# Optimization experiments

Measured on AMD Instinct MI355X. Metric: run time of the kernel, lower is better.

## Reference

```python
import jax, jax.numpy as jnp
import numpy as np

NUM_NODES = 200000
NUM_EDGES = 640000
RANK = 16
EMBED_DIM = 128


def setup_inputs() -> dict:
    key = jax.random.key(0)
    k1, k2, k3 = jax.random.split(key, 3)
    U = jax.random.normal(k1, (NUM_NODES, RANK), dtype=jnp.float32)
    V = jax.random.normal(k2, (RANK, EMBED_DIM), dtype=jnp.float32)
    edge_index = jax.random.randint(k3, (2, NUM_EDGES), 0, NUM_NODES, dtype=jnp.int64)
    return {"U": U, "V": V, "edge_index": edge_index}


def reference(U, V, edge_index):
    # Low-rank projection: [N, r] @ [r, d] -> [N, d]
    embeddings = jnp.matmul(U, V)
    src, dst = edge_index[0], edge_index[1]
    # Mean aggregation (PyG MessagePassing aggr='mean', source_to_target):
    # gather messages from source nodes, segment-mean into destination nodes.
    msgs = embeddings[src]  # [E, d]
    summed = jax.ops.segment_sum(msgs, dst, num_segments=NUM_NODES)  # [N, d]
    counts = jax.ops.segment_sum(jnp.ones((edge_index.shape[1],), dtype=embeddings.dtype),
                                 dst, num_segments=NUM_NODES)  # [N]
    denom = jnp.maximum(counts, 1.0)  # isolated nodes -> 0 output (scatter-mean semantics)
    return summed / denom[:, None]
```

## Files before the change

### kernel.cpp

```cpp
#include <hip/hip_runtime.h>

#define RANK 16
#define EMBED_DIM 128
#define CAP 16

typedef float floatx4 __attribute__((ext_vector_type(4)));

__global__ __launch_bounds__(256) void fill_slots(
        const int* __restrict__ eiw,
        int* __restrict__ cnt,
        int* __restrict__ ovfcnt,
        int* __restrict__ slots,
        int* __restrict__ ovf,
        int E, int nwords) {
    __shared__ int iflag;
    if (threadIdx.x == 0) iflag = 0;
    __syncthreads();
    {
        int w = 2 * threadIdx.x + 1;
        unsigned int v = (w < nwords) ? ((const unsigned int*)eiw)[w] : 0u;
        if (v) atomicOr(&iflag, 1);
    }
    __syncthreads();
    const bool is32 = (iflag != 0);

    const int base = (blockIdx.x * 256 + threadIdx.x) * 2;
    if (base >= E) return;

    int srcs[2], dsts[2];
    int ne;
    if ((E & 1) == 0 && base + 1 < E) {
        ne = 2;
        if (is32) {
            int2 s = *(const int2*)(eiw + base);
            int2 d = *(const int2*)(eiw + E + base);
            srcs[0] = s.x; srcs[1] = s.y;
            dsts[0] = d.x; dsts[1] = d.y;
        } else {
            int4 sv = *(const int4*)(eiw + 2 * base);
            int4 dv = *(const int4*)(eiw + 2 * (E + base));
            srcs[0] = sv.x; srcs[1] = sv.z;
            dsts[0] = dv.x; dsts[1] = dv.z;
        }
    } else {
        ne = 0;
        for (int e = base; e < E && e < base + 2; ++e, ++ne) {
            srcs[ne] = is32 ? eiw[e] : eiw[2 * e];
            dsts[ne] = is32 ? eiw[E + e] : eiw[2 * (E + e)];
        }
    }

#pragma unroll
    for (int j = 0; j < 2; ++j) {
        if (j >= ne) break;
        int dst = dsts[j];
        int pos = atomicAdd(&cnt[dst], 1);
        if (pos < CAP) {
            slots[(size_t)dst * CAP + pos] = srcs[j];
        } else {
            int o = atomicAdd(ovfcnt, 1);
            ovf[2 * o]     = srcs[j];
            ovf[2 * o + 1] = dst;
        }
    }
}

__global__ __launch_bounds__(256) void gather_project(
        const float* __restrict__ U,
        const float* __restrict__ V,
        const int* __restrict__ cnt,
        const int* __restrict__ slots,
        const int* __restrict__ ovfcnt,
        const int* __restrict__ ovf,
        float* __restrict__ out, int N, int ntiles) {
    __shared__ float4 Vs4[RANK * EMBED_DIM / 4];
    __shared__ float accs[32][RANK];
    __shared__ float sinv[32];
    __shared__ int   scnt[32];
    __shared__ int4  sslot4[32 * CAP / 4];

    const int t = threadIdx.x;
    const float4* V4 = (const float4*)V;
    Vs4[t]       = V4[t];
    Vs4[t + 256] = V4[t + 256];

    const int g = t >> 4;
    const int j = t & 15;
    const int q = t & 31;
    const int w = t >> 5;
    const int* sslot = (const int*)sslot4;

    for (int tile = blockIdx.x; tile < ntiles; tile += gridDim.x) {
        const int n0 = tile * 32;
        __syncthreads();

        if (t < 32) {
            int n = n0 + t;
            int c = (n < N) ? cnt[n] : 0;
            scnt[t] = c;
            sinv[t] = 1.0f / fmaxf((float)c, 1.0f);
        }
        if (t < 128) {
            const int4* g4 = (const int4*)(slots + (size_t)n0 * CAP);
            if (n0 + (t >> 2) < N) sslot4[t] = g4[t];
        }
        __syncthreads();

#pragma unroll
        for (int half = 0; half < 2; ++half) {
            int nd = half * 16 + g;
            int n = n0 + nd;
            float acc = 0.f;
            if (n < N) {
                int deg = scnt[nd];
                int k = deg < CAP ? deg : CAP;
                const int* sl = sslot + nd * CAP;
                for (int e = 0; e < k; e += 4) {
                    int s0 = sl[e];
                    int s1 = (e + 1 < k) ? sl[e + 1] : s0;
                    int s2 = (e + 2 < k) ? sl[e + 2] : s0;
                    int s3 = (e + 3 < k) ? sl[e + 3] : s0;
                    float u0 = U[(size_t)s0 * RANK + j];
                    float u1 = U[(size_t)s1 * RANK + j];
                    float u2 = U[(size_t)s2 * RANK + j];
                    float u3 = U[(size_t)s3 * RANK + j];
                    acc += u0;
                    acc += (e + 1 < k) ? u1 : 0.f;
                    acc += (e + 2 < k) ? u2 : 0.f;
                    acc += (e + 3 < k) ? u3 : 0.f;
                }
                if (deg > CAP) {
                    int m = *ovfcnt;
                    for (int i = 0; i < m; ++i)
                        if (ovf[2 * i + 1] == n)
                            acc += U[(size_t)ovf[2 * i] * RANK + j];
                }
            }
            accs[nd][j] = acc;
        }
        __syncthreads();

#pragma unroll
        for (int r = 0; r < 4; ++r) {
            int nd = 4 * w + r;
            float4 a4 = make_float4(0.f, 0.f, 0.f, 0.f);
#pragma unroll
            for (int k = 0; k < RANK; ++k) {
                float a = accs[nd][k];
                float4 v = Vs4[k * 32 + q];
                a4.x = fmaf(a, v.x, a4.x);
                a4.y = fmaf(a, v.y, a4.y);
                a4.z = fmaf(a, v.z, a4.z);
                a4.w = fmaf(a, v.w, a4.w);
            }
            float s = sinv[nd];
            int n = n0 + nd;
            if (n < N) {
                floatx4 o;
                o.x = a4.x * s; o.y = a4.y * s; o.z = a4.z * s; o.w = a4.w * s;
                __builtin_nontemporal_store(
                    o, (floatx4*)out + (size_t)n * (EMBED_DIM / 4) + q);
            }
        }
    }
}

extern "C" void kernel_launch(void* const* d_in, const int* in_sizes, int n_in,
                              void* d_out, int out_size, void* d_ws, size_t ws_size,
                              hipStream_t stream) {
    const float* U = (const float*)d_in[0];
    const float* V = (const float*)d_in[1];
    const int* EI = (const int*)d_in[2];
    float* out = (float*)d_out;

    const int N = in_sizes[0] / RANK;
    const int E = in_sizes[2] / 2;
    const int nwords = in_sizes[2];

    int* wsI = (int*)d_ws;
    int* cnt = wsI;
    int* ovfcnt = wsI + N;
    const int slots_off = (N + 1 + 15) & ~15;
    int* slots = wsI + slots_off;
    int* ovf = slots + (size_t)N * CAP;

    (void)hipMemsetAsync(d_ws, 0, (size_t)(N + 1) * sizeof(int), stream);

    fill_slots<<<(E / 2 + 255) / 256, 256, 0, stream>>>(
        EI, cnt, ovfcnt, slots, ovf, E, nwords);

    const int ntiles = (N + 31) / 32;
    const int nblk = ntiles < 2560 ? ntiles : 2560;
    gather_project<<<nblk, 256, 0, stream>>>(
        U, V, cnt, slots, ovfcnt, ovf, out, N, ntiles);
}
```

Before: 180.4 us.

## Vectorize U-row gathers with float4 loads and shuffle-reduce, 64 nodes per block

The gather phase now has each thread load a float4 quarter of a U row. Four edges per node are processed in parallel by 16 lanes, and the partial sums are combined with xor shuffles. This replaces the old scalar per-lane loads and aims to cut load instruction count and raise memory-level parallelism. The persistent grid-stride loop is replaced by one 64-node tile per block, with a larger grid. This drops loop overhead and syncthreads per tile, but it reloads V into shared memory in every block.

Result: faster. 173.2 us, median of 2 (-4.0%).

```diff
diff --git a/kernel.cpp b/kernel.cpp
--- a/kernel.cpp
+++ b/kernel.cpp
@@ -5,6 +5,15 @@
 #define CAP 16
 
 typedef float floatx4 __attribute__((ext_vector_type(4)));
+
+__device__ inline floatx4 shflx4(floatx4 v, int mask) {
+    floatx4 r;
+    r.x = __shfl_xor(v.x, mask);
+    r.y = __shfl_xor(v.y, mask);
+    r.z = __shfl_xor(v.z, mask);
+    r.w = __shfl_xor(v.w, mask);
+    return r;
+}
 
 __global__ __launch_bounds__(256) void fill_slots(
         const int* __restrict__ eiw,
@@ -72,95 +81,93 @@
         const int* __restrict__ slots,
         const int* __restrict__ ovfcnt,
         const int* __restrict__ ovf,
-        float* __restrict__ out, int N, int ntiles) {
-    __shared__ float4 Vs4[RANK * EMBED_DIM / 4];
-    __shared__ float accs[32][RANK];
-    __shared__ float sinv[32];
-    __shared__ int   scnt[32];
-    __shared__ int4  sslot4[32 * CAP / 4];
+        float* __restrict__ out, int N) {
+    __shared__ float4  Vs4[RANK * EMBED_DIM / 4];
+    __shared__ floatx4 accs4[64][4];
+    __shared__ float   sinv[64];
+    __shared__ int     scnt[64];
+    __shared__ int4    sslot4[64 * CAP / 4];
 
     const int t = threadIdx.x;
     const float4* V4 = (const float4*)V;
     Vs4[t]       = V4[t];
     Vs4[t + 256] = V4[t + 256];
 
-    const int g = t >> 4;
-    const int j = t & 15;
+    const int n0 = blockIdx.x * 64;
+
+    if (t < 64) {
+        int n = n0 + t;
+        int c = (n < N) ? cnt[n] : 0;
+        scnt[t] = c;
+        sinv[t] = 1.0f / fmaxf((float)c, 1.0f);
+    }
+    {
+        const int4* g4 = (const int4*)(slots + (size_t)n0 * CAP);
+        if (n0 + (t >> 2) < N) sslot4[t] = g4[t];
+    }
+    __syncthreads();
+
+    const int* sslot = (const int*)sslot4;
+    const int g    = t >> 4;
+    const int l    = t & 15;
+    const int es   = l >> 2;
+    const int quad = l & 3;
+
+#pragma unroll
+    for (int half = 0; half < 4; ++half) {
+        int nd = half * 16 + g;
+        int n = n0 + nd;
+        int deg = scnt[nd];
+        int k = deg < CAP ? deg : CAP;
+        const int* sl = sslot + nd * CAP;
+        floatx4 a = (floatx4)0.f;
+        for (int e = 0; e < k; e += 8) {
+            int e0 = e + es;
+            int e1 = e + 4 + es;
+            int i0 = e0 < k ? e0 : k - 1;
+            int i1 = e1 < k ? e1 : k - 1;
+            int s0 = sl[i0];
+            int s1 = sl[i1];
+            floatx4 u0 = *(const floatx4*)(U + (size_t)s0 * RANK + 4 * quad);
+            floatx4 u1 = *(const floatx4*)(U + (size_t)s1 * RANK + 4 * quad);
+            if (e0 < k) a += u0;
+            if (e1 < k) a += u1;
+        }
+        a += shflx4(a, 4);
+        a += shflx4(a, 8);
+        if (l < 4) {
+            if (deg > CAP) {
+                int m = *ovfcnt;
+                for (int i = 0; i < m; ++i)
+                    if (ovf[2 * i + 1] == n)
+                        a += *(const floatx4*)(U + (size_t)ovf[2 * i] * RANK + 4 * l);
+            }
+            accs4[nd][l] = a;
+        }
+    }
+    __syncthreads();
+
+    const float* accsf = (const float*)accs4;
     const int q = t & 31;
     const int w = t >> 5;
-    const int* sslot = (const int*)sslot4;
-
-    for (int tile = blockIdx.x; tile < ntiles; tile += gridDim.x) {
-        const int n0 = tile * 32;
-        __syncthreads();
-
-        if (t < 32) {
-            int n = n0 + t;
-            int c = (n < N) ? cnt[n] : 0;
-            scnt[t] = c;
-            sinv[t] = 1.0f / fmaxf((float)c, 1.0f);
-        }
-        if (t < 128) {
-            const int4* g4 = (const int4*)(slots + (size_t)n0 * CAP);
-            if (n0 + (t >> 2) < N) sslot4[t] = g4[t];
-        }
-        __syncthreads();
-
-#pragma unroll
-        for (int half = 0; half < 2; ++half) {
-            int nd = half * 16 + g;
-            int n = n0 + nd;
-            float acc = 0.f;
-            if (n < N) {
-                int deg = scnt[nd];
-                int k = deg < CAP ? deg : CAP;
-                const int* sl = sslot + nd * CAP;
-                for (int e = 0; e < k; e += 4) {
-                    int s0 = sl[e];
-                    int s1 = (e + 1 < k) ? sl[e + 1] : s0;
-                    int s2 = (e + 2 < k) ? sl[e + 2] : s0;
-                    int s3 = (e + 3 < k) ? sl[e + 3] : s0;
-                    float u0 = U[(size_t)s0 * RANK + j];
-                    float u1 = U[(size_t)s1 * RANK + j];
-                    float u2 = U[(size_t)s2 * RANK + j];
-                    float u3 = U[(size_t)s3 * RANK + j];
-                    acc += u0;
-                    acc += (e + 1 < k) ? u1 : 0.f;
-                    acc += (e + 2 < k) ? u2 : 0.f;
-                    acc += (e + 3 < k) ? u3 : 0.f;
-                }
-                if (deg > CAP) {
-                    int m = *ovfcnt;
-                    for (int i = 0; i < m; ++i)
-                        if (ovf[2 * i + 1] == n)
-                            acc += U[(size_t)ovf[2 * i] * RANK + j];
-                }
-            }
-            accs[nd][j] = acc;
-        }
-        __syncthreads();
-
-#pragma unroll
-        for (int r = 0; r < 4; ++r) {
-            int nd = 4 * w + r;
-            float4 a4 = make_float4(0.f, 0.f, 0.f, 0.f);
-#pragma unroll
-            for (int k = 0; k < RANK; ++k) {
-                float a = accs[nd][k];
-                float4 v = Vs4[k * 32 + q];
-                a4.x = fmaf(a, v.x, a4.x);
-                a4.y = fmaf(a, v.y, a4.y);
-                a4.z = fmaf(a, v.z, a4.z);
-                a4.w = fmaf(a, v.w, a4.w);
-            }
-            float s = sinv[nd];
-            int n = n0 + nd;
-            if (n < N) {
-                floatx4 o;
-                o.x = a4.x * s; o.y = a4.y * s; o.z = a4.z * s; o.w = a4.w * s;
-                __builtin_nontemporal_store(
-                    o, (floatx4*)out + (size_t)n * (EMBED_DIM / 4) + q);
-            }
+#pragma unroll
+    for (int r = 0; r < 8; ++r) {
+        int nd = w * 8 + r;
+        floatx4 o = (floatx4)0.f;
+#pragma unroll
+        for (int k = 0; k < RANK; ++k) {
+            float a = accsf[nd * 16 + k];
+            float4 v = Vs4[k * 32 + q];
+            o.x = fmaf(a, v.x, o.x);
+            o.y = fmaf(a, v.y, o.y);
+            o.z = fmaf(a, v.z, o.z);
+            o.w = fmaf(a, v.w, o.w);
+        }
+        int n = n0 + nd;
+        if (n < N) {
+            o *= sinv[nd];
+            __builtin_nontemporal_store(
+                o, (floatx4*)out + (size_t)n * (EMBED_DIM / 4) + q);
         }
     }
 }
@@ -189,8 +196,6 @@
     fill_slots<<<(E / 2 + 255) / 256, 256, 0, stream>>>(
         EI, cnt, ovfcnt, slots, ovf, E, nwords);
 
-    const int ntiles = (N + 31) / 32;
-    const int nblk = ntiles < 2560 ? ntiles : 2560;
-    gather_project<<<nblk, 256, 0, stream>>>(
-        U, V, cnt, slots, ovfcnt, ovf, out, N, ntiles);
-}
+    gather_project<<<(N + 63) / 64, 256, 0, stream>>>(
+        U, V, cnt, slots, ovfcnt, ovf, out, N);
+}
```
